# Kernel tuning notes

Hardware: AMD Instinct MI355X
Metric: run time of the kernel (lower is better)

The kernel has to match this reference:

```python
import jax, jax.numpy as jnp
import numpy as np

B, S, HID = 2, 2048, 2048
H, D = 16, 128        # num_heads, kv_channels
LAYER_IDX = 4
MASK_VALUE = -10000.0


def setup_inputs() -> dict:
    key = jax.random.key(0)
    ks = jax.random.split(key, 5)
    hidden_states = jax.random.normal(ks[0], (B, S, HID), dtype=jnp.float32)
    # causal mask, broadcastable to [B, q, H, k] per torch.where(mask, w, mask_value)
    causal = jnp.tril(jnp.ones((S, S), dtype=bool))
    attention_mask = jnp.broadcast_to(causal[None, :, None, :], (B, S, 1, S))
    Wq = jax.random.normal(ks[1], (HID, H * D), dtype=jnp.float32) * (HID ** -0.5)
    bq = jnp.zeros((H * D,), dtype=jnp.float32)
    Wkv = jax.random.normal(ks[2], (HID, 2 * D), dtype=jnp.float32) * (HID ** -0.5)
    bkv = jnp.zeros((2 * D,), dtype=jnp.float32)
    Wp = jax.random.normal(ks[3], (H * D, HID), dtype=jnp.float32) * ((H * D) ** -0.5)
    bp = jnp.zeros((HID,), dtype=jnp.float32)
    return {"hidden_states": hidden_states, "attention_mask": attention_mask,
            "Wq": Wq, "bq": bq, "Wkv": Wkv, "bkv": bkv, "Wp": Wp, "bp": bp}


def reference(hidden_states, attention_mask, Wq, bq, Wkv, bkv, Wp, bp):
    # projections
    q = hidden_states @ Wq + bq                      # [B,S,H*D]
    kv = hidden_states @ Wkv + bkv                   # [B,S,2D]
    k, v = kv[..., :D], kv[..., D:]                  # shared single K/V head [B,S,D]
    qh = q.reshape(B, S, H, D)
    # baddbmm with alpha = 1/(layer_idx * sqrt(D))
    scale_factor = (1.0 / LAYER_IDX) / (D ** 0.5)
    scores = jnp.einsum('bqhd,bkd->bqhk', qh, k) * scale_factor  # [B,q,H,k]
    # upcast softmax with unscale = layer_idx, masked with -1e4
    scores = scores.astype(jnp.float32) * LAYER_IDX
    scores = jnp.where(attention_mask, scores, MASK_VALUE)
    weights = jax.nn.softmax(scores, axis=-1).astype(hidden_states.dtype)
    attn = jnp.einsum('bqhk,bkd->bqhd', weights, v).reshape(B, S, H * D)
    out = attn @ Wp + bp
    return out
```

## Files before the change

kernel.cpp:

```cpp
#include <hip/hip_runtime.h>

#define DEVI __device__ __forceinline__

typedef unsigned int u32;
typedef unsigned short u16;

constexpr int Bc = 2, Sc = 2048, HIDc = 2048, Hc = 16, Dc = 128;
constexpr int Mrows = Bc * Sc;
constexpr float SCALE = 0.08838834764831845f;
constexpr float M0 = 16.0f;

typedef float f32x4 __attribute__((ext_vector_type(4)));
typedef __bf16 bf16x8 __attribute__((ext_vector_type(8)));

DEVI float bf2f(u16 v) { return __builtin_bit_cast(float, (u32)v << 16); }
DEVI u16 f2bf(float x) {
  u32 u = __builtin_bit_cast(u32, x);
  u32 r = (u + 0x7fffu + ((u >> 16) & 1u)) >> 16;
  return (u16)r;
}

DEVI void async16(void* lds, const void* g) {
  __builtin_amdgcn_global_load_lds((const __attribute__((address_space(1))) void*)g,
                                   (__attribute__((address_space(3))) void*)lds,
                                   16, 0, 0);
}

constexpr int PRE_BLOCKS = 6289;
constexpr int TS = 66;

DEVI void do_transpose64(const void* in, u16* out, int R, int C, int c0, int r0, bool bf,
                         u16* tile, int tid) {
  const int cg = (tid & 7) * 8, ry = tid >> 3;
#pragma unroll
  for (int p = 0; p < 2; ++p) {
    int r = ry + p * 32;
    size_t idx = (size_t)(r0 + r) * C + (c0 + cg);
    u16 tmp[8];
    if (bf) {
      *(uint4*)tmp = *(const uint4*)&((const u16*)in)[idx];
    } else {
      const float* f = (const float*)in + idx;
#pragma unroll
      for (int j = 0; j < 8; ++j) tmp[j] = f2bf(f[j]);
    }
    *(uint4*)&tile[r * TS + cg] = *(const uint4*)tmp;
  }
  __syncthreads();
  const int rx = (tid & 7) * 8, cy = tid >> 3;
#pragma unroll
  for (int p = 0; p < 2; ++p) {
    int c = cy + p * 32;
    u16 tmp[8];
#pragma unroll
    for (int j = 0; j < 8; ++j) tmp[j] = tile[(rx + j) * TS + c];
    *(uint4*)&out[(size_t)(c0 + c) * R + r0 + rx] = *(const uint4*)tmp;
  }
}

__global__ __launch_bounds__(256) void pre_kernel(const void* __restrict__ hs,
                                                  const void* __restrict__ Wq,
                                                  const void* __restrict__ bq,
                                                  const void* __restrict__ Wkv,
                                                  const void* __restrict__ bkv,
                                                  const void* __restrict__ Wp,
                                                  const void* __restrict__ bp,
                                                  u16* __restrict__ HSb, u16* __restrict__ WqT,
                                                  u16* __restrict__ WkvT, u16* __restrict__ WpT,
                                                  u16* __restrict__ biasB, int* __restrict__ flag) {
  __shared__ int cnt;
  __shared__ u16 tile[64 * TS];
  const int tid = threadIdx.x, bx = blockIdx.x;
  if (tid == 0) cnt = 0;
  __syncthreads();
  int ok = 0;
  const u32* hw = (const u32*)hs;
  for (int i = tid; i < 512; i += 256) {
    u32 lo = hw[i] & 0xffffu;
    u32 e = (lo >> 7) & 0xffu;
    if (lo == 0u || (e >= 118u && e <= 134u)) ok++;
  }
  atomicAdd(&cnt, ok);
  __syncthreads();
  const bool bf = cnt > 256;
  if (bx == 0 && tid == 0) *flag = bf ? 1 : 0;

  if (bx < 4096) {
    if (bf) return;
    int i = (bx * 256 + tid) * 8;
    const float* f = (const float*)hs;
    u16 tmp[8];
#pragma unroll
    for (int j = 0; j < 8; ++j) tmp[j] = f2bf(f[i + j]);
    *(uint4*)&HSb[i] = *(const uint4*)tmp;
  } else if (bx < 5120) {
    int t = bx - 4096;
    do_transpose64(Wq, WqT, 2048, 2048, (t & 31) * 64, (t >> 5) * 64, bf, tile, tid);
  } else if (bx < 5248) {
    int t = bx - 5120;
    do_transpose64(Wkv, WkvT, 2048, 256, (t & 3) * 64, (t >> 2) * 64, bf, tile, tid);
  } else if (bx < 6272) {
    int t = bx - 5248;
    do_transpose64(Wp, WpT, 2048, 2048, (t & 31) * 64, (t >> 5) * 64, bf, tile, tid);
  } else {
    int i = (bx - 6272) * 256 + tid;
    if (i < 4352) {
      const void* src;
      int j;
      if (i < 2048) { src = bq; j = i; }
      else if (i < 2304) { src = bkv; j = i - 2048; }
      else { src = bp; j = i - 2304; }
      biasB[i] = bf ? ((const u16*)src)[j] : f2bf(((const float*)src)[j]);
    }
  }
}

__global__ __launch_bounds__(512, 4) void gemm_bt(const u16* __restrict__ A0,
                                                  const u16* __restrict__ A1,
                                                  const u16* __restrict__ BT,
                                                  const u16* __restrict__ bias,
                                                  void* __restrict__ C,
                                                  int M, int N, int K,
                                                  const int* __restrict__ flag,
                                                  int mode) {
  __shared__ __align__(16) u16 As[2][128 * 32];
  __shared__ __align__(16) u16 Bs[2][128 * 32];
  const u16* __restrict__ A = (*flag != 0) ? A1 : A0;
  const int tid = threadIdx.x;
  const int bm = blockIdx.x, bn = blockIdx.y;
  const int wave = tid >> 6, lane = tid & 63;
  const int wm = (wave & 3) * 32, wn = (wave >> 2) * 64;
  const int lr = lane & 15, kq = lane >> 4;
  f32x4 acc[2][4] = {};
  const size_t a_base = (size_t)bm * 128 * K;
  const size_t b_base = (size_t)bn * 128 * K;

#define STAGE(k0, buf)                                                             \
  {                                                                                \
    int r = tid >> 2, c = tid & 3;                                                 \
    int gc = (c ^ (r & 3)) << 3;                                                   \
    async16(&As[buf][tid * 8], A + a_base + (size_t)r * K + (k0) + gc);            \
    async16(&Bs[buf][tid * 8], BT + b_base + (size_t)r * K + (k0) + gc);           \
  }

  STAGE(0, 0);
  const int nsteps = K >> 5;
  for (int s = 0; s < nsteps; ++s) {
    const int cur = s & 1;
    asm volatile("s_waitcnt vmcnt(0)" ::: "memory");
    asm volatile("s_barrier" ::: "memory");
    if (s + 1 < nsteps) STAGE((s + 1) << 5, cur ^ 1);
    bf16x8 af[2], bfr[4];
#pragma unroll
    for (int i = 0; i < 2; ++i) {
      int ra = wm + i * 16 + lr;
      af[i] = *(const bf16x8*)&As[cur][ra * 32 + ((kq ^ (ra & 3)) << 3)];
    }
#pragma unroll
    for (int i = 0; i < 4; ++i) {
      int rb = wn + i * 16 + lr;
      bfr[i] = *(const bf16x8*)&Bs[cur][rb * 32 + ((kq ^ (rb & 3)) << 3)];
    }
#pragma unroll
    for (int mi = 0; mi < 2; ++mi)
#pragma unroll
      for (int ni = 0; ni < 4; ++ni)
        acc[mi][ni] = __builtin_amdgcn_mfma_f32_16x16x32_bf16(af[mi], bfr[ni], acc[mi][ni], 0, 0, 0);
  }
#undef STAGE

  if (mode == 3) {
    u16* Qout = (u16*)C;
    u16* KsG = Qout + (size_t)4096 * 2048;
    u16* VtG = KsG + (size_t)4096 * 128;
    const bool isQ = (bn < 16);
#pragma unroll
    for (int mi = 0; mi < 2; ++mi)
#pragma unroll
      for (int ni = 0; ni < 4; ++ni) {
        int col = bn * 128 + wn + ni * 16 + lr;
        float bv = bf2f(bias[col]);
#pragma unroll
        for (int rr = 0; rr < 4; ++rr) {
          int row = bm * 128 + wm + mi * 16 + kq * 4 + rr;
          u16 v = f2bf(acc[mi][ni][rr] + bv);
          if (isQ) {
            Qout[(size_t)row * 2048 + col] = v;
          } else {
            int c2 = col - 2048;
            if (c2 < 128) {
              int d = c2;
              KsG[(size_t)row * 128 + (((d >> 3) ^ (row & 15)) << 3) + (d & 7)] = v;
            } else {
              int d = c2 - 128, bb = row >> 11, s = row & 2047;
              VtG[((size_t)(bb * 128 + d)) * 2048 + (s & ~63) +
                  ((((s >> 3) & 7) ^ (d & 7)) << 3) + (s & 7)] = v;
            }
          }
        }
      }
    return;
  }
  const bool out16 = (mode == 0) || (*flag != 0);
#pragma unroll
  for (int mi = 0; mi < 2; ++mi)
#pragma unroll
    for (int ni = 0; ni < 4; ++ni) {
      int col = bn * 128 + wn + ni * 16 + lr;
      float bv = bf2f(bias[col]);
#pragma unroll
      for (int rr = 0; rr < 4; ++rr) {
        int row = bm * 128 + wm + mi * 16 + kq * 4 + rr;
        float v = acc[mi][ni][rr] + bv;
        size_t idx = (size_t)row * N + col;
        if (out16) ((u16*)C)[idx] = f2bf(v);
        else ((float*)C)[idx] = v;
      }
    }
}

__global__ __launch_bounds__(512, 4) void flash_mfma(const u16* __restrict__ Q,
                                                     const u16* __restrict__ KsG,
                                                     const u16* __restrict__ VtG,
                                                     u16* __restrict__ O) {
  __shared__ __align__(16) u16 Ks[2][64 * 128];
  __shared__ __align__(16) u16 Vt[2][128 * 64];
  __shared__ __align__(16) u16 Ps[8][16 * 64];
  const int pairidx = blockIdx.x, h = blockIdx.y, b = blockIdx.z;
  const int tid = threadIdx.x;
  const int wave = tid >> 6, lane = tid & 63;
  const int lr = lane & 15, kq = lane >> 4;
  const int qw = wave & 3, grp = wave >> 2;
  const int qt = grp ? (31 - pairidx) : pairidx;
  const int kmax = qt * 64;
  const int kmaxblk = (31 - pairidx) * 64;

  bf16x8 qf[4];
  const u16* qbase = Q + ((size_t)(b * 2048 + qt * 64 + qw * 16 + lr)) * 2048 + h * 128;
#pragma unroll
  for (int kk = 0; kk < 4; ++kk)
    qf[kk] = *(const bf16x8*)(qbase + kk * 32 + kq * 8);
  f32x4 of[8] = {};
  float lsum[4] = {0.f, 0.f, 0.f, 0.f};
  const int srow = qt * 64 + qw * 16 + kq * 4;

  {
    const u16* g = KsG + ((size_t)(b * 2048)) * 128;
#pragma unroll
    for (int it = 0; it < 2; ++it)
      async16(&Ks[0][(it * 512 + tid) * 8], g + (it * 512 + tid) * 8);
    const size_t vbase = ((size_t)b * 128) * 2048;
#pragma unroll
    for (int it = 0; it < 2; ++it) {
      int ch = it * 512 + tid;
      async16(&Vt[0][ch * 8], VtG + vbase + (size_t)(ch >> 3) * 2048 + (ch & 7) * 8);
    }
  }

  for (int k0 = 0; k0 <= kmaxblk; k0 += 64) {
    const int cur = (k0 >> 6) & 1;
    asm volatile("s_waitcnt vmcnt(0)" ::: "memory");
    asm volatile("s_barrier" ::: "memory");
    if (k0 + 64 <= kmaxblk) {
      const int nxt = cur ^ 1;
      const u16* g = KsG + ((size_t)(b * 2048 + k0 + 64)) * 128;
#pragma unroll
      for (int it = 0; it < 2; ++it)
        async16(&Ks[nxt][(it * 512 + tid) * 8], g + (it * 512 + tid) * 8);
      const size_t vbase = ((size_t)b * 128) * 2048 + k0 + 64;
#pragma unroll
      for (int it = 0; it < 2; ++it) {
        int ch = it * 512 + tid;
        async16(&Vt[nxt][ch * 8], VtG + vbase + (size_t)(ch >> 3) * 2048 + (ch & 7) * 8);
      }
    }
    if (k0 > kmax) continue;

    const bool diag = (k0 == kmax);
    f32x4 sf[4] = {};
#pragma unroll
    for (int nt = 0; nt < 4; ++nt) {
      int keyl = nt * 16 + lr;
#pragma unroll
      for (int kk = 0; kk < 4; ++kk) {
        const bf16x8 kf = *(const bf16x8*)&Ks[cur][keyl * 128 + ((((kk << 2) + kq) ^ lr) << 3)];
        sf[nt] = __builtin_amdgcn_mfma_f32_16x16x32_bf16(qf[kk], kf, sf[nt], 0, 0, 0);
      }
    }
#pragma unroll
    for (int nt = 0; nt < 4; ++nt) {
      int t = k0 + nt * 16 + lr;
#pragma unroll
      for (int r = 0; r < 4; ++r) {
        float v = fmaf(sf[nt][r], SCALE, -M0);
        if (diag && t > srow + r) v = -1e30f;
        float p = __expf(v);
        lsum[r] += p;
        int row = kq * 4 + r;
        Ps[wave][row * 64 + (((nt * 2 + (lr >> 3)) ^ (row & 7)) << 3) + (lr & 7)] = f2bf(p);
      }
    }
#pragma unroll
    for (int ks = 0; ks < 2; ++ks) {
      const bf16x8 pf = *(const bf16x8*)&Ps[wave][lr * 64 + ((((ks << 2) + kq) ^ (lr & 7)) << 3)];
#pragma unroll
      for (int dt = 0; dt < 8; ++dt) {
        int d = dt * 16 + lr;
        const bf16x8 vf = *(const bf16x8*)&Vt[cur][d * 64 + ((((ks << 2) + kq) ^ (d & 7)) << 3)];
        of[dt] = __builtin_amdgcn_mfma_f32_16x16x32_bf16(pf, vf, of[dt], 0, 0, 0);
      }
    }
  }
  float linv[4];
#pragma unroll
  for (int r = 0; r < 4; ++r) {
    float l = lsum[r];
    l += __shfl_xor(l, 1);
    l += __shfl_xor(l, 2);
    l += __shfl_xor(l, 4);
    l += __shfl_xor(l, 8);
    linv[r] = 1.f / l;
  }
  u16* obase = O + ((size_t)(b * 2048 + qt * 64 + qw * 16 + kq * 4)) * 2048 + h * 128;
#pragma unroll
  for (int dt = 0; dt < 8; ++dt)
#pragma unroll
    for (int r = 0; r < 4; ++r)
      obase[(size_t)r * 2048 + dt * 16 + lr] = f2bf(of[dt][r] * linv[r]);
}

extern "C" void kernel_launch(void* const* d_in, const int* in_sizes, int n_in,
                              void* d_out, int out_size, void* d_ws, size_t ws_size,
                              hipStream_t stream) {
  (void)in_sizes; (void)n_in; (void)out_size; (void)ws_size;
  const void* hs  = d_in[0];
  const void* Wq  = d_in[2];
  const void* bq  = d_in[3];
  const void* Wkv = d_in[4];
  const void* bkv = d_in[5];
  const void* Wp  = d_in[6];
  const void* bp  = d_in[7];

  char* ws = (char*)d_ws;
  int* flag  = (int*)(ws + 0);
  u16* HSb   = (u16*)(ws + 256);
  u16* WqT   = (u16*)(ws + 16777472);
  u16* WkvT  = (u16*)(ws + 25166080);
  u16* WpT   = (u16*)(ws + 26214656);
  u16* biasB = (u16*)(ws + 34603264);
  u16* Qb    = (u16*)(ws + 34611968);
  u16* KsG   = (u16*)(ws + 51389184);
  u16* VtG   = (u16*)(ws + 52437760);
  u16* ATTNb = (u16*)(ws + 53486336);

  pre_kernel<<<PRE_BLOCKS, 256, 0, stream>>>(hs, Wq, bq, Wkv, bkv, Wp, bp,
                                             HSb, WqT, WkvT, WpT, biasB, flag);
  gemm_bt<<<dim3(32, 18), 512, 0, stream>>>(HSb, (const u16*)hs, WqT, biasB, Qb,
                                            4096, 2304, 2048, flag, 3);
  flash_mfma<<<dim3(16, 16, 2), 512, 0, stream>>>(Qb, KsG, VtG, ATTNb);
  gemm_bt<<<dim3(32, 16), 512, 0, stream>>>(ATTNb, ATTNb, WpT, biasB + 2304, d_out,
                                            4096, 2048, 2048, flag, 1);
}
```

Before: 316.2 us.

## Switch flash attention to 32x32x16 MFMA with four waves of 32 query rows

The attention kernel now uses 32x32x16 bf16 MFMA instructions instead of 16x16x32 ones. Each block drops from 8 waves of 16 query rows to 4 waves of 32 rows, so the launch and load loops shrink to 256 threads. Larger MFMA tiles mean each wave reads fewer K/V fragments from LDS per output element and spends more of its time in matrix instructions. The cost is fewer waves per block and per CU to hide latency, plus more accumulator registers per wave (16-wide row sums and outputs).

Measured after the change: 401.9 us. +27.1%, slower.

```diff
diff --git a/kernel.cpp b/kernel.cpp
--- a/kernel.cpp
+++ b/kernel.cpp
@@ -11,6 +11,7 @@
 constexpr float M0 = 16.0f;
 
 typedef float f32x4 __attribute__((ext_vector_type(4)));
+typedef float f32x16 __attribute__((ext_vector_type(16)));
 typedef __bf16 bf16x8 __attribute__((ext_vector_type(8)));
 
 DEVI float bf2f(u16 v) { return __builtin_bit_cast(float, (u32)v << 16); }
@@ -219,40 +220,42 @@
     }
 }
 
-__global__ __launch_bounds__(512, 4) void flash_mfma(const u16* __restrict__ Q,
-                                                     const u16* __restrict__ KsG,
-                                                     const u16* __restrict__ VtG,
-                                                     u16* __restrict__ O) {
+__global__ __launch_bounds__(256) void flash_mfma(const u16* __restrict__ Q,
+                                                  const u16* __restrict__ KsG,
+                                                  const u16* __restrict__ VtG,
+                                                  u16* __restrict__ O) {
   __shared__ __align__(16) u16 Ks[2][64 * 128];
   __shared__ __align__(16) u16 Vt[2][128 * 64];
-  __shared__ __align__(16) u16 Ps[8][16 * 64];
+  __shared__ __align__(16) u16 Ps[4][32 * 64];
   const int pairidx = blockIdx.x, h = blockIdx.y, b = blockIdx.z;
   const int tid = threadIdx.x;
   const int wave = tid >> 6, lane = tid & 63;
-  const int lr = lane & 15, kq = lane >> 4;
-  const int qw = wave & 3, grp = wave >> 2;
+  const int ln31 = lane & 31, khalf = lane >> 5;
+  const int qhalf = wave & 1, grp = wave >> 1;
   const int qt = grp ? (31 - pairidx) : pairidx;
   const int kmax = qt * 64;
   const int kmaxblk = (31 - pairidx) * 64;
 
-  bf16x8 qf[4];
-  const u16* qbase = Q + ((size_t)(b * 2048 + qt * 64 + qw * 16 + lr)) * 2048 + h * 128;
-#pragma unroll
-  for (int kk = 0; kk < 4; ++kk)
-    qf[kk] = *(const bf16x8*)(qbase + kk * 32 + kq * 8);
-  f32x4 of[8] = {};
-  float lsum[4] = {0.f, 0.f, 0.f, 0.f};
-  const int srow = qt * 64 + qw * 16 + kq * 4;
+  bf16x8 qf[8];
+  const u16* qbase = Q + ((size_t)(b * 2048 + qt * 64 + qhalf * 32 + ln31)) * 2048 + h * 128;
+#pragma unroll
+  for (int kc = 0; kc < 8; ++kc)
+    qf[kc] = *(const bf16x8*)(qbase + kc * 16 + khalf * 8);
+  f32x16 of[4] = {};
+  float lsum[16];
+#pragma unroll
+  for (int i = 0; i < 16; ++i) lsum[i] = 0.f;
+  const int srow_base = qt * 64 + qhalf * 32;
 
   {
     const u16* g = KsG + ((size_t)(b * 2048)) * 128;
 #pragma unroll
-    for (int it = 0; it < 2; ++it)
-      async16(&Ks[0][(it * 512 + tid) * 8], g + (it * 512 + tid) * 8);
+    for (int it = 0; it < 4; ++it)
+      async16(&Ks[0][(it * 256 + tid) * 8], g + (it * 256 + tid) * 8);
     const size_t vbase = ((size_t)b * 128) * 2048;
 #pragma unroll
-    for (int it = 0; it < 2; ++it) {
-      int ch = it * 512 + tid;
+    for (int it = 0; it < 4; ++it) {
+      int ch = it * 256 + tid;
       async16(&Vt[0][ch * 8], VtG + vbase + (size_t)(ch >> 3) * 2048 + (ch & 7) * 8);
     }
   }
@@ -265,68 +268,74 @@
       const int nxt = cur ^ 1;
       const u16* g = KsG + ((size_t)(b * 2048 + k0 + 64)) * 128;
 #pragma unroll
-      for (int it = 0; it < 2; ++it)
-        async16(&Ks[nxt][(it * 512 + tid) * 8], g + (it * 512 + tid) * 8);
+      for (int it = 0; it < 4; ++it)
+        async16(&Ks[nxt][(it * 256 + tid) * 8], g + (it * 256 + tid) * 8);
       const size_t vbase = ((size_t)b * 128) * 2048 + k0 + 64;
 #pragma unroll
-      for (int it = 0; it < 2; ++it) {
-        int ch = it * 512 + tid;
+      for (int it = 0; it < 4; ++it) {
+        int ch = it * 256 + tid;
         async16(&Vt[nxt][ch * 8], VtG + vbase + (size_t)(ch >> 3) * 2048 + (ch & 7) * 8);
       }
     }
     if (k0 > kmax) continue;
 
     const bool diag = (k0 == kmax);
-    f32x4 sf[4] = {};
-#pragma unroll
-    for (int nt = 0; nt < 4; ++nt) {
-      int keyl = nt * 16 + lr;
-#pragma unroll
-      for (int kk = 0; kk < 4; ++kk) {
-        const bf16x8 kf = *(const bf16x8*)&Ks[cur][keyl * 128 + ((((kk << 2) + kq) ^ lr) << 3)];
-        sf[nt] = __builtin_amdgcn_mfma_f32_16x16x32_bf16(qf[kk], kf, sf[nt], 0, 0, 0);
-      }
-    }
-#pragma unroll
-    for (int nt = 0; nt < 4; ++nt) {
-      int t = k0 + nt * 16 + lr;
-#pragma unroll
-      for (int r = 0; r < 4; ++r) {
-        float v = fmaf(sf[nt][r], SCALE, -M0);
-        if (diag && t > srow + r) v = -1e30f;
+    f32x16 sf[2] = {};
+#pragma unroll
+    for (int nt = 0; nt < 2; ++nt) {
+      int key = nt * 32 + ln31;
+#pragma unroll
+      for (int kc = 0; kc < 8; ++kc) {
+        const bf16x8 kf =
+            *(const bf16x8*)&Ks[cur][key * 128 + (((2 * kc + khalf) ^ (key & 15)) << 3)];
+        sf[nt] = __builtin_amdgcn_mfma_f32_32x32x16_bf16(qf[kc], kf, sf[nt], 0, 0, 0);
+      }
+    }
+#pragma unroll
+    for (int nt = 0; nt < 2; ++nt) {
+      int t = k0 + nt * 32 + ln31;
+#pragma unroll
+      for (int reg = 0; reg < 16; ++reg) {
+        int row = (reg & 3) + 8 * (reg >> 2) + 4 * khalf;
+        float v = fmaf(sf[nt][reg], SCALE, -M0);
+        if (diag && t > srow_base + row) v = -1e30f;
         float p = __expf(v);
-        lsum[r] += p;
-        int row = kq * 4 + r;
-        Ps[wave][row * 64 + (((nt * 2 + (lr >> 3)) ^ (row & 7)) << 3) + (lr & 7)] = f2bf(p);
-      }
-    }
-#pragma unroll
-    for (int ks = 0; ks < 2; ++ks) {
-      const bf16x8 pf = *(const bf16x8*)&Ps[wave][lr * 64 + ((((ks << 2) + kq) ^ (lr & 7)) << 3)];
-#pragma unroll
-      for (int dt = 0; dt < 8; ++dt) {
-        int d = dt * 16 + lr;
-        const bf16x8 vf = *(const bf16x8*)&Vt[cur][d * 64 + ((((ks << 2) + kq) ^ (d & 7)) << 3)];
-        of[dt] = __builtin_amdgcn_mfma_f32_16x16x32_bf16(pf, vf, of[dt], 0, 0, 0);
-      }
-    }
-  }
-  float linv[4];
-#pragma unroll
-  for (int r = 0; r < 4; ++r) {
-    float l = lsum[r];
+        lsum[reg] += p;
+        Ps[wave][row * 64 + ((((nt << 2) + (ln31 >> 3)) ^ (row & 7)) << 3) + (lane & 7)] = f2bf(p);
+      }
+    }
+#pragma unroll
+    for (int ks = 0; ks < 4; ++ks) {
+      const bf16x8 pf =
+          *(const bf16x8*)&Ps[wave][ln31 * 64 + (((2 * ks + khalf) ^ (ln31 & 7)) << 3)];
+#pragma unroll
+      for (int dt = 0; dt < 4; ++dt) {
+        int d = dt * 32 + ln31;
+        const bf16x8 vf =
+            *(const bf16x8*)&Vt[cur][d * 64 + (((2 * ks + khalf) ^ (d & 7)) << 3)];
+        of[dt] = __builtin_amdgcn_mfma_f32_32x32x16_bf16(pf, vf, of[dt], 0, 0, 0);
+      }
+    }
+  }
+  float linv[16];
+#pragma unroll
+  for (int reg = 0; reg < 16; ++reg) {
+    float l = lsum[reg];
     l += __shfl_xor(l, 1);
     l += __shfl_xor(l, 2);
     l += __shfl_xor(l, 4);
     l += __shfl_xor(l, 8);
-    linv[r] = 1.f / l;
-  }
-  u16* obase = O + ((size_t)(b * 2048 + qt * 64 + qw * 16 + kq * 4)) * 2048 + h * 128;
-#pragma unroll
-  for (int dt = 0; dt < 8; ++dt)
-#pragma unroll
-    for (int r = 0; r < 4; ++r)
-      obase[(size_t)r * 2048 + dt * 16 + lr] = f2bf(of[dt][r] * linv[r]);
+    l += __shfl_xor(l, 16);
+    linv[reg] = 1.f / l;
+  }
+  u16* obase = O + ((size_t)(b * 2048 + srow_base)) * 2048 + h * 128;
+#pragma unroll
+  for (int dt = 0; dt < 4; ++dt)
+#pragma unroll
+    for (int reg = 0; reg < 16; ++reg) {
+      int row = (reg & 3) + 8 * (reg >> 2) + 4 * khalf;
+      obase[(size_t)row * 2048 + dt * 32 + ln31] = f2bf(of[dt][reg] * linv[reg]);
+    }
 }
 
 extern "C" void kernel_launch(void* const* d_in, const int* in_sizes, int n_in,
@@ -357,7 +366,7 @@
                                              HSb, WqT, WkvT, WpT, biasB, flag);
   gemm_bt<<<dim3(32, 18), 512, 0, stream>>>(HSb, (const u16*)hs, WqT, biasB, Qb,
                                             4096, 2304, 2048, flag, 3);
-  flash_mfma<<<dim3(16, 16, 2), 512, 0, stream>>>(Qb, KsG, VtG, ATTNb);
+  flash_mfma<<<dim3(16, 16, 2), 256, 0, stream>>>(Qb, KsG, VtG, ATTNb);
   gemm_bt<<<dim3(32, 16), 512, 0, stream>>>(ATTNb, ATTNb, WpT, biasB + 2304, d_out,
                                             4096, 2048, 2048, flag, 1);
 }
```
